# Kernel tuning notes

Hardware: AMD Instinct MI355X
Metric: run time of the kernel (lower is better)

Reference implementation:

```python
import jax, jax.numpy as jnp
import numpy as np

B, S, HIDDEN = 2, 2048, 2048
HEADS, GROUPS, KVC = 16, 4, 128
HPG = HEADS // GROUPS  # heads per group
LAYER_INDEX = 2
SOFTMAX_SCALE = KVC ** -0.5
ROPE_THETA = 10000.0


def _rope_tables(seq_len, dim, dtype=jnp.float32):
    inv_freq = 1.0 / (ROPE_THETA ** (jnp.arange(0, dim, 2, dtype=jnp.float32) / dim))
    t = jnp.arange(seq_len, dtype=jnp.float32)
    freqs = jnp.outer(t, inv_freq)  # [S, dim/2]
    return jnp.cos(freqs).astype(dtype), jnp.sin(freqs).astype(dtype)


def _apply_rope(x, cos, sin):
    # x: [b, s, h, d]; rotate-half (GPT-NeoX style)
    d2 = x.shape[-1] // 2
    x1, x2 = x[..., :d2], x[..., d2:]
    c = cos[None, :, None, :]
    s = sin[None, :, None, :]
    return jnp.concatenate([x1 * c - x2 * s, x2 * c + x1 * s], axis=-1)


def setup_inputs() -> dict:
    key = jax.random.key(0)
    k1, k2, k3, k4 = jax.random.split(key, 4)
    std = HIDDEN ** -0.5
    return {
        "x": jax.random.normal(k1, (B, S, HIDDEN), dtype=jnp.float32),
        "w_q": jax.random.normal(k2, (HIDDEN, HEADS * KVC), dtype=jnp.float32) * std,
        "w_kv": jax.random.normal(k3, (HIDDEN, 2 * GROUPS * KVC), dtype=jnp.float32) * std,
        "w_dense": jax.random.normal(k4, (HEADS * KVC, HIDDEN), dtype=jnp.float32) * std,
    }


def reference(x, w_q, w_kv, w_dense):
    b, s, _ = x.shape
    # QKV projections
    q = (x @ w_q).reshape(b, s, HEADS, KVC)                 # [b,s,H,d]
    kv = (x @ w_kv).reshape(b, s, 2, GROUPS, KVC)
    k, v = kv[:, :, 0], kv[:, :, 1]                          # [b,s,G,d]
    # Rotary embeddings on q and k
    cos, sin = _rope_tables(s, KVC, x.dtype)
    q = _apply_rope(q, cos, sin)
    k = _apply_rope(k, cos, sin)
    # GQA attention with per-layer scaling trick:
    # scores computed at scale/softmax of layer_index, cast fp32, rescaled back.
    qg = q.reshape(b, s, GROUPS, HPG, KVC)
    scores = jnp.einsum("bqghd,bkgd->bghqk", qg, k) * (SOFTMAX_SCALE / LAYER_INDEX)
    scores = scores.astype(jnp.float32) * LAYER_INDEX
    # causal mask
    causal = jnp.tril(jnp.ones((s, s), dtype=bool))
    mask_value = jnp.finfo(jnp.float32).min
    scores = jnp.where(causal[None, None, None, :, :], scores, mask_value)
    probs = jax.nn.softmax(scores, axis=-1).astype(x.dtype)  # dropout p=0 (eval)
    ctx = jnp.einsum("bghqk,bkgd->bqghd", probs, v).reshape(b, s, HEADS * KVC)
    return ctx @ w_dense
```

## Files before the change

kernel.cpp:

```cpp
#include <hip/hip_runtime.h>
#include <hip/hip_bf16.h>
#include <stdint.h>

typedef unsigned short u16;
typedef __bf16 bf16x8 __attribute__((ext_vector_type(8)));
typedef float f32x4 __attribute__((ext_vector_type(4)));

#define S_LEN 2048
#define BATCH 2
#define NHEADS 16
#define NGROUPS 4
#define DHEAD 128
#define QKV_W 3072

__device__ __forceinline__ float bf2f(u16 u) {
  union { uint32_t i; float f; } v; v.i = ((uint32_t)u) << 16; return v.f;
}
__device__ __forceinline__ u16 f2bf(float f) {
  union { float f; uint32_t i; } v; v.f = f;
  uint32_t r = v.i + 0x7FFF + ((v.i >> 16) & 1);
  return (u16)(r >> 16);
}
__device__ __forceinline__ void llds16(const void* g, void* l) {
  __builtin_amdgcn_global_load_lds(
      (const __attribute__((address_space(1))) uint32_t*)g,
      (__attribute__((address_space(3))) uint32_t*)l, 16, 0, 0);
}

__device__ __forceinline__ void store_out(u16* C, long i, float v) { C[i] = f2bf(v); }
__device__ __forceinline__ void store_out(float* C, long i, float v) { C[i] = v; }

__global__ void rope_tables_k(float* __restrict__ cosT, float* __restrict__ sinT) {
  int i = blockIdx.x * 256 + threadIdx.x;
  int s = i >> 6, j = i & 63;
  float inv = exp2f(-(float)j * 0.20762050593045983f);
  float ang = (float)s * inv;
  float sv, cv;
  sincosf(ang, &sv, &cv);
  cosT[i] = cv; sinT[i] = sv;
}

__global__ void cvt_f32_bf16(const float* __restrict__ in, u16* __restrict__ out) {
  long i = ((long)blockIdx.x * 256 + threadIdx.x) * 4;
  float4 v = *(const float4*)(in + i);
  ushort4 o;
  o.x = f2bf(v.x); o.y = f2bf(v.y); o.z = f2bf(v.z); o.w = f2bf(v.w);
  *(ushort4*)(out + i) = o;
}

__global__ void transpose_f32_bf16(const float* __restrict__ in, u16* __restrict__ out,
                                   int R, int C) {
  __shared__ u16 tile[32][33];
  int c0 = blockIdx.x * 32, r0 = blockIdx.y * 32;
  int tx = threadIdx.x, ty = threadIdx.y;
  for (int i = 0; i < 32; i += 8)
    tile[ty + i][tx] = f2bf(in[(long)(r0 + ty + i) * C + c0 + tx]);
  __syncthreads();
  for (int i = 0; i < 32; i += 8)
    out[(long)(c0 + ty + i) * R + r0 + tx] = tile[tx][ty + i];
}

template <typename OutT>
__global__ __launch_bounds__(256) void gemm_bt(
    const u16* __restrict__ A, const u16* __restrict__ Bt, OutT* __restrict__ C,
    int M, int N, int K) {
  __shared__ __align__(16) __bf16 As[128 * 32];
  __shared__ __align__(16) __bf16 Bs[128 * 32];
  const int tid = threadIdx.x;
  const int wv = tid >> 6;
  const int lane = tid & 63;
  const int quad = lane >> 4;
  const int l16 = lane & 15;
  const int bm = blockIdx.y * 128;
  const int bn = blockIdx.x * 128;

  f32x4 acc[4][4] = {};

  const int arow = wv * 32 + (lane >> 2);
  const int kseg = (lane & 3) * 8;
  const int wm = (wv >> 1) * 64, wn = (wv & 1) * 64;

  for (int k0 = 0; k0 < K; k0 += 32) {
    __syncthreads();
    const u16* ga0 = A + (long)(bm + arow) * K + k0 + kseg;
    llds16(ga0, &As[arow * 32 + kseg]);
    llds16(ga0 + (long)16 * K, &As[(arow + 16) * 32 + kseg]);
    const u16* gb0 = Bt + (long)(bn + arow) * K + k0 + kseg;
    llds16(gb0, &Bs[arow * 32 + kseg]);
    llds16(gb0 + (long)16 * K, &Bs[(arow + 16) * 32 + kseg]);
    __syncthreads();

    bf16x8 af[4], bfr[4];
#pragma unroll
    for (int mt = 0; mt < 4; ++mt)
      af[mt] = *(const bf16x8*)&As[(wm + mt * 16 + l16) * 32 + quad * 8];
#pragma unroll
    for (int nt = 0; nt < 4; ++nt)
      bfr[nt] = *(const bf16x8*)&Bs[(wn + nt * 16 + l16) * 32 + quad * 8];
#pragma unroll
    for (int mt = 0; mt < 4; ++mt)
#pragma unroll
      for (int nt = 0; nt < 4; ++nt)
        acc[mt][nt] = __builtin_amdgcn_mfma_f32_16x16x32_bf16(
            af[mt], bfr[nt], acc[mt][nt], 0, 0, 0);
  }

#pragma unroll
  for (int mt = 0; mt < 4; ++mt)
#pragma unroll
    for (int nt = 0; nt < 4; ++nt)
#pragma unroll
      for (int r = 0; r < 4; ++r) {
        int row = bm + wm + mt * 16 + quad * 4 + r;
        int col = bn + wn + nt * 16 + l16;
        store_out(C, (long)row * N + col, acc[mt][nt][r]);
      }
}

__global__ void rope_q_k(u16* __restrict__ qkv, const float* __restrict__ cosT,
                         const float* __restrict__ sinT) {
  long i = (long)blockIdx.x * 256 + threadIdx.x;
  int j = i & 63;
  long rest = i >> 6;
  int h = rest & 15;
  long bs = rest >> 4;
  int s = bs & (S_LEN - 1);
  long base = bs * QKV_W + h * DHEAD + j;
  float x1 = bf2f(qkv[base]), x2 = bf2f(qkv[base + 64]);
  float c = cosT[s * 64 + j], sn = sinT[s * 64 + j];
  qkv[base] = f2bf(x1 * c - x2 * sn);
  qkv[base + 64] = f2bf(x2 * c + x1 * sn);
}

__global__ void rope_k_k(const u16* __restrict__ qkv, u16* __restrict__ Kb,
                         const float* __restrict__ cosT, const float* __restrict__ sinT) {
  long i = (long)blockIdx.x * 256 + threadIdx.x;
  int j = i & 63;
  long rest = i >> 6;
  int g = rest & 3;
  long bs = rest >> 2;
  int s = bs & (S_LEN - 1);
  int b = (int)(bs >> 11);
  long src = bs * QKV_W + 2048 + g * 128 + j;
  float x1 = bf2f(qkv[src]), x2 = bf2f(qkv[src + 64]);
  float c = cosT[s * 64 + j], sn = sinT[s * 64 + j];
  long dst = ((long)(b * NGROUPS + g) * S_LEN + s) * DHEAD + j;
  Kb[dst] = f2bf(x1 * c - x2 * sn);
  Kb[dst + 64] = f2bf(x2 * c + x1 * sn);
}

__global__ void v_trans_k(const u16* __restrict__ qkv, u16* __restrict__ Vt) {
  __shared__ u16 tile[32][33];
  int s0 = blockIdx.x * 32, d0 = blockIdx.y * 32;
  int bg = blockIdx.z;
  int b = bg >> 2, g = bg & 3;
  int tx = threadIdx.x, ty = threadIdx.y;
  for (int i = 0; i < 32; i += 8) {
    long s = s0 + ty + i;
    tile[ty + i][tx] = qkv[((long)b * S_LEN + s) * QKV_W + 2560 + g * 128 + d0 + tx];
  }
  __syncthreads();
  for (int i = 0; i < 32; i += 8) {
    int d = d0 + ty + i;
    Vt[((long)(b * NGROUPS + g) * DHEAD + d) * S_LEN + s0 + tx] = tile[tx][ty + i];
  }
}

__global__ __launch_bounds__(256, 2) void attn_k5(
    const u16* __restrict__ Q,
    const u16* __restrict__ Kb,
    const u16* __restrict__ Vt,
    u16* __restrict__ ctx) {
  __shared__ __align__(16) __bf16 Ks[2][64 * 128];
  __shared__ __align__(16) __bf16 Vts[2][128 * 64];
  __shared__ __align__(16) __bf16 Ps[64 * 64];

  const int h = blockIdx.y, b = blockIdx.z, g = h >> 2;
  const int tid = threadIdx.x, wv = tid >> 6, lane = tid & 63;
  const int quad = lane >> 4, l16 = lane & 15;
  const float SCALE = 0.08838834764831845f;

  const long kbase = (long)(b * NGROUPS + g) * S_LEN * DHEAD;
  const long vbase = (long)(b * NGROUPS + g) * DHEAD * S_LEN;

  const int krow_off = lane >> 4;
  const int vrow_off = lane >> 3;

  const __bf16 oneb = (__bf16)((l16 == 0) ? 1.0f : 0.0f);
  const bf16x8 bones = {oneb, oneb, oneb, oneb, oneb, oneb, oneb, oneb};

  for (int pass = 0; pass < 2; ++pass) {
    const int tile = pass == 0 ? (int)blockIdx.x : 31 - (int)blockIdx.x;
    const int q0 = tile * 64;
    const int nch = tile + 1;

    bf16x8 aq[4];
    {
      const u16* qp = Q + (long)(b * S_LEN + q0 + wv * 16 + l16) * QKV_W + h * DHEAD + quad * 8;
#pragma unroll
      for (int ds = 0; ds < 4; ++ds)
        aq[ds] = *(const bf16x8*)(qp + ds * 32);
    }

#pragma unroll
    for (int i = 0; i < 4; ++i) {
      int r0 = wv * 16 + i * 4;
      int row = r0 + krow_off;
      int c = l16 ^ (row & 15);
      llds16(Kb + kbase + (long)row * DHEAD + c * 8, &Ks[0][r0 * 128 + lane * 8]);
    }
#pragma unroll
    for (int i = 0; i < 4; ++i) {
      int d0 = wv * 32 + i * 8;
      int row = d0 + vrow_off;
      int c = (lane & 7) ^ (row & 7);
      llds16(Vt + vbase + (long)row * S_LEN + c * 8, &Vts[0][d0 * 64 + lane * 8]);
    }
    __syncthreads();

    f32x4 Oacc[9] = {};

    for (int kc = 0; kc < nch; ++kc) {
      const int cur = kc & 1;
      if (kc + 1 < nch) {
        const int nxt = cur ^ 1;
#pragma unroll
        for (int i = 0; i < 4; ++i) {
          int r0 = wv * 16 + i * 4;
          int row = r0 + krow_off;
          int c = l16 ^ (row & 15);
          llds16(Kb + kbase + (long)((kc + 1) * 64 + row) * DHEAD + c * 8,
                 &Ks[nxt][r0 * 128 + lane * 8]);
        }
#pragma unroll
        for (int i = 0; i < 4; ++i) {
          int d0 = wv * 32 + i * 8;
          int row = d0 + vrow_off;
          int c = (lane & 7) ^ (row & 7);
          llds16(Vt + vbase + (long)row * S_LEN + (kc + 1) * 64 + c * 8,
                 &Vts[nxt][d0 * 64 + lane * 8]);
        }
      }

      f32x4 sacc[4] = {};
#pragma unroll
      for (int ds = 0; ds < 4; ++ds) {
        int pos0 = ((ds * 4 + quad) ^ l16) * 8;
#pragma unroll
        for (int nt = 0; nt < 4; ++nt) {
          bf16x8 bk = *(const bf16x8*)&Ks[cur][(nt * 16 + l16) * 128 + pos0];
          sacc[nt] = __builtin_amdgcn_mfma_f32_16x16x32_bf16(aq[ds], bk, sacc[nt], 0, 0, 0);
        }
      }

#pragma unroll
      for (int nt = 0; nt < 4; ++nt)
#pragma unroll
        for (int r = 0; r < 4; ++r) {
          int qrow = q0 + wv * 16 + quad * 4 + r;
          int key = kc * 64 + nt * 16 + l16;
          float p = (key <= qrow) ? __expf(sacc[nt][r] * SCALE) : 0.f;
          int qlocal = quad * 4 + r;
          int chunk = nt * 2 + (l16 >> 3);
          int pos = chunk ^ (qlocal & 7);
          Ps[(wv * 16 + qlocal) * 64 + pos * 8 + (l16 & 7)] = (__bf16)p;
        }

      bf16x8 ap[2];
#pragma unroll
      for (int kf = 0; kf < 2; ++kf) {
        int pos = ((kf * 4 + quad) ^ (l16 & 7)) * 8;
        ap[kf] = *(const bf16x8*)&Ps[(wv * 16 + l16) * 64 + pos];
      }
#pragma unroll
      for (int nt = 0; nt < 8; ++nt)
#pragma unroll
        for (int kf = 0; kf < 2; ++kf) {
          int pos = ((kf * 4 + quad) ^ (l16 & 7)) * 8;
          bf16x8 bv = *(const bf16x8*)&Vts[cur][(nt * 16 + l16) * 64 + pos];
          Oacc[nt] = __builtin_amdgcn_mfma_f32_16x16x32_bf16(ap[kf], bv, Oacc[nt], 0, 0, 0);
        }
      Oacc[8] = __builtin_amdgcn_mfma_f32_16x16x32_bf16(ap[0], bones, Oacc[8], 0, 0, 0);
      Oacc[8] = __builtin_amdgcn_mfma_f32_16x16x32_bf16(ap[1], bones, Oacc[8], 0, 0, 0);

      __syncthreads();
    }

    float lsum[4];
#pragma unroll
    for (int r = 0; r < 4; ++r)
      lsum[r] = __shfl(Oacc[8][r], quad << 4, 64);

    const long obase = ((long)(b * S_LEN + q0 + wv * 16) * NHEADS + h) * DHEAD;
#pragma unroll
    for (int nt = 0; nt < 8; ++nt)
#pragma unroll
      for (int r = 0; r < 4; ++r) {
        int lrow = quad * 4 + r;
        ctx[obase + (long)lrow * NHEADS * DHEAD + nt * 16 + l16] =
            f2bf(Oacc[nt][r] / lsum[r]);
      }
  }
}

extern "C" void kernel_launch(void* const* d_in, const int* in_sizes, int n_in,
                              void* d_out, int out_size, void* d_ws, size_t ws_size,
                              hipStream_t stream) {
  const float* x   = (const float*)d_in[0];
  const float* wq  = (const float*)d_in[1];
  const float* wkv = (const float*)d_in[2];
  const float* wd  = (const float*)d_in[3];
  float* out = (float*)d_out;

  char* ws = (char*)d_ws;
  float* cosT  = (float*)(ws + 0);
  float* sinT  = (float*)(ws + 524288);
  u16* wqkvT = (u16*)(ws + 1048576);
  u16* wdT   = (u16*)(ws + 13631488);
  u16* xb    = (u16*)(ws + 22020096);
  u16* qkv   = (u16*)(ws + 38797312);
  u16* Kb    = (u16*)(ws + 63963136);
  u16* Vt    = (u16*)(ws + 68157440);
  u16* ctx   = (u16*)(ws + 72351744);

  rope_tables_k<<<512, 256, 0, stream>>>(cosT, sinT);
  cvt_f32_bf16<<<8192, 256, 0, stream>>>(x, xb);
  transpose_f32_bf16<<<dim3(64, 64), dim3(32, 8), 0, stream>>>(wq, wqkvT, 2048, 2048);
  transpose_f32_bf16<<<dim3(32, 64), dim3(32, 8), 0, stream>>>(wkv, wqkvT + (long)2048 * 2048, 2048, 1024);
  transpose_f32_bf16<<<dim3(64, 64), dim3(32, 8), 0, stream>>>(wd, wdT, 2048, 2048);

  gemm_bt<u16><<<dim3(24, 32), 256, 0, stream>>>(xb, wqkvT, qkv, 4096, 3072, 2048);

  rope_q_k<<<16384, 256, 0, stream>>>(qkv, cosT, sinT);
  rope_k_k<<<4096, 256, 0, stream>>>(qkv, Kb, cosT, sinT);
  v_trans_k<<<dim3(64, 4, 8), dim3(32, 8), 0, stream>>>(qkv, Vt);

  attn_k5<<<dim3(16, 16, 2), 256, 0, stream>>>(qkv, Kb, Vt, ctx);

  gemm_bt<float><<<dim3(16, 32), 256, 0, stream>>>(ctx, wdT, out, 4096, 2048, 2048);
}
```

Before: 313.3 us.

## Replace GEMM with 256x256 double-buffered, swizzled 8-wave pipelined kernel

Replaces the 128x128 single-buffered GEMM with a 512-thread kernel computing 256x256 tiles. K-steps are 64 wide, held in double-buffered LDS with an XOR-swizzled layout, and staged with global_load_lds prefetch two steps ahead. Each K-step is split into four phases with barriers and s_setprio so loads overlap MFMA work, and the workgroup index is remapped for cache locality. The aim is to hide global memory latency and raise reuse, at the cost of fewer workgroups (192 and 128 tiles on the MI355X's CUs) and heavier register and LDS use.

```diff
diff --git a/kernel.cpp b/kernel.cpp
--- a/kernel.cpp
+++ b/kernel.cpp
@@ -60,60 +60,162 @@
     out[(long)(c0 + ty + i) * R + r0 + tx] = tile[tx][ty + i];
 }
 
+
+#define GFENCE() asm volatile("" ::: "memory")
+#define MIDBAR() do { GFENCE(); __builtin_amdgcn_s_barrier(); \
+    asm volatile("s_waitcnt lgkmcnt(0)" ::: "memory"); } while (0)
+#define ENDBAR() do { GFENCE(); __builtin_amdgcn_s_barrier(); GFENCE(); } while (0)
+
+__device__ __forceinline__ bf16x8 frag_ld(const __bf16* h, int wrow, int kk, int quad) {
+  int b = ((wrow & 15) << 6) | (quad << 4);
+  b ^= ((wrow >> 3) & 1) << 5;
+  int off = ((((wrow >> 4) << 1) | kk) << 10) | b;
+  return *(const bf16x8*)((const char*)h + off);
+}
+
+__device__ __forceinline__ void stage_half(const u16* __restrict__ g, int K,
+                                           __bf16* lhalf, int wv, int lane) {
+  int bsrc = (lane << 4) ^ (((lane >> 5) & 1) << 5);
+  int r = bsrc >> 6, c = (bsrc & 63) >> 1;
+  int cb = (wv & 1) << 5;
+  llds16(g + (long)((wv >> 1) * 16 + r) * K + cb + c,
+         lhalf + wv * 512 + lane * 8);
+  llds16(g + (long)((4 + (wv >> 1)) * 16 + r) * K + cb + c,
+         lhalf + 4096 + wv * 512 + lane * 8);
+}
+
 template <typename OutT>
-__global__ __launch_bounds__(256) void gemm_bt(
+__global__ __launch_bounds__(512) void gemm_bt8(
     const u16* __restrict__ A, const u16* __restrict__ Bt, OutT* __restrict__ C,
     int M, int N, int K) {
-  __shared__ __align__(16) __bf16 As[128 * 32];
-  __shared__ __align__(16) __bf16 Bs[128 * 32];
+  __shared__ __align__(16) __bf16 lds[2][2][16384];
   const int tid = threadIdx.x;
-  const int wv = tid >> 6;
-  const int lane = tid & 63;
-  const int quad = lane >> 4;
-  const int l16 = lane & 15;
-  const int bm = blockIdx.y * 128;
-  const int bn = blockIdx.x * 128;
-
-  f32x4 acc[4][4] = {};
-
-  const int arow = wv * 32 + (lane >> 2);
-  const int kseg = (lane & 3) * 8;
-  const int wm = (wv >> 1) * 64, wn = (wv & 1) * 64;
-
-  for (int k0 = 0; k0 < K; k0 += 32) {
-    __syncthreads();
-    const u16* ga0 = A + (long)(bm + arow) * K + k0 + kseg;
-    llds16(ga0, &As[arow * 32 + kseg]);
-    llds16(ga0 + (long)16 * K, &As[(arow + 16) * 32 + kseg]);
-    const u16* gb0 = Bt + (long)(bn + arow) * K + k0 + kseg;
-    llds16(gb0, &Bs[arow * 32 + kseg]);
-    llds16(gb0 + (long)16 * K, &Bs[(arow + 16) * 32 + kseg]);
-    __syncthreads();
-
-    bf16x8 af[4], bfr[4];
-#pragma unroll
-    for (int mt = 0; mt < 4; ++mt)
-      af[mt] = *(const bf16x8*)&As[(wm + mt * 16 + l16) * 32 + quad * 8];
+  const int wv = tid >> 6, lane = tid & 63;
+  const int quad = lane >> 4, l16 = lane & 15;
+  const int wr = wv >> 2, wc = wv & 3;
+
+  const int nwg = gridDim.x * gridDim.y;
+  const int orig = blockIdx.y * gridDim.x + blockIdx.x;
+  const int swz = (orig & 7) * (nwg >> 3) + (orig >> 3);
+  const int bx = swz % gridDim.x, by = swz / gridDim.x;
+  const int bm = by * 256, bn = bx * 256;
+
+  const u16* Abase = A + (long)bm * K;
+  const u16* Bbase = Bt + (long)bn * K;
+  const int NT = K >> 6;
+
+  f32x4 acc[8][4] = {};
+
+  stage_half(Abase, K, &lds[0][0][0], wv, lane);
+  stage_half(Abase + (long)128 * K, K, &lds[0][0][8192], wv, lane);
+  stage_half(Bbase, K, &lds[0][1][0], wv, lane);
+  stage_half(Bbase + (long)128 * K, K, &lds[0][1][8192], wv, lane);
+  stage_half(Abase + 64, K, &lds[1][0][0], wv, lane);
+  stage_half(Abase + (long)128 * K + 64, K, &lds[1][0][8192], wv, lane);
+  stage_half(Bbase + 64, K, &lds[1][1][0], wv, lane);
+  stage_half(Bbase + (long)128 * K + 64, K, &lds[1][1][8192], wv, lane);
+  asm volatile("s_waitcnt vmcnt(8)" ::: "memory");
+  __builtin_amdgcn_s_barrier();
+  GFENCE();
+
+  for (int kt = 0; kt < NT; ++kt) {
+    const int buf = kt & 1;
+    const __bf16* Ah = &lds[buf][0][wr * 8192];
+    const __bf16* Bh = &lds[buf][1][(wc >> 1) * 8192];
+    const int brow0 = (wc & 1) << 6;
+    const bool pre = (kt + 2 < NT);
+    bf16x8 aF[4][2], bF[4][2];
+
+#pragma unroll
+    for (int m = 0; m < 4; ++m) {
+      aF[m][0] = frag_ld(Ah, m * 16 + l16, 0, quad);
+      aF[m][1] = frag_ld(Ah, m * 16 + l16, 1, quad);
+    }
+#pragma unroll
+    for (int n = 0; n < 2; ++n) {
+      bF[n][0] = frag_ld(Bh, brow0 + n * 16 + l16, 0, quad);
+      bF[n][1] = frag_ld(Bh, brow0 + n * 16 + l16, 1, quad);
+    }
+    MIDBAR();
+    __builtin_amdgcn_s_setprio(1);
+#pragma unroll
+    for (int m = 0; m < 4; ++m)
+#pragma unroll
+      for (int n = 0; n < 2; ++n) {
+        acc[m][n] = __builtin_amdgcn_mfma_f32_16x16x32_bf16(aF[m][0], bF[n][0], acc[m][n], 0, 0, 0);
+        acc[m][n] = __builtin_amdgcn_mfma_f32_16x16x32_bf16(aF[m][1], bF[n][1], acc[m][n], 0, 0, 0);
+      }
+    __builtin_amdgcn_s_setprio(0);
+    ENDBAR();
+
+#pragma unroll
+    for (int n = 2; n < 4; ++n) {
+      bF[n][0] = frag_ld(Bh, brow0 + n * 16 + l16, 0, quad);
+      bF[n][1] = frag_ld(Bh, brow0 + n * 16 + l16, 1, quad);
+    }
+    MIDBAR();
+    __builtin_amdgcn_s_setprio(1);
+#pragma unroll
+    for (int m = 0; m < 4; ++m)
+#pragma unroll
+      for (int n = 2; n < 4; ++n) {
+        acc[m][n] = __builtin_amdgcn_mfma_f32_16x16x32_bf16(aF[m][0], bF[n][0], acc[m][n], 0, 0, 0);
+        acc[m][n] = __builtin_amdgcn_mfma_f32_16x16x32_bf16(aF[m][1], bF[n][1], acc[m][n], 0, 0, 0);
+      }
+    __builtin_amdgcn_s_setprio(0);
+    ENDBAR();
+
+#pragma unroll
+    for (int m = 0; m < 4; ++m) {
+      aF[m][0] = frag_ld(Ah, 64 + m * 16 + l16, 0, quad);
+      aF[m][1] = frag_ld(Ah, 64 + m * 16 + l16, 1, quad);
+    }
+    if (pre) {
+      const u16* p = Bbase + (long)(kt + 2) * 64;
+      stage_half(p, K, &lds[buf][1][0], wv, lane);
+      stage_half(p + (long)128 * K, K, &lds[buf][1][8192], wv, lane);
+    }
+    MIDBAR();
+    __builtin_amdgcn_s_setprio(1);
+#pragma unroll
+    for (int m = 0; m < 4; ++m)
+#pragma unroll
+      for (int n = 2; n < 4; ++n) {
+        acc[4 + m][n] = __builtin_amdgcn_mfma_f32_16x16x32_bf16(aF[m][0], bF[n][0], acc[4 + m][n], 0, 0, 0);
+        acc[4 + m][n] = __builtin_amdgcn_mfma_f32_16x16x32_bf16(aF[m][1], bF[n][1], acc[4 + m][n], 0, 0, 0);
+      }
+    __builtin_amdgcn_s_setprio(0);
+    ENDBAR();
+
+    if (pre) {
+      const u16* p = Abase + (long)(kt + 2) * 64;
+      stage_half(p, K, &lds[buf][0][0], wv, lane);
+      stage_half(p + (long)128 * K, K, &lds[buf][0][8192], wv, lane);
+    }
+    MIDBAR();
+    __builtin_amdgcn_s_setprio(1);
+#pragma unroll
+    for (int m = 0; m < 4; ++m)
+#pragma unroll
+      for (int n = 0; n < 2; ++n) {
+        acc[4 + m][n] = __builtin_amdgcn_mfma_f32_16x16x32_bf16(aF[m][0], bF[n][0], acc[4 + m][n], 0, 0, 0);
+        acc[4 + m][n] = __builtin_amdgcn_mfma_f32_16x16x32_bf16(aF[m][1], bF[n][1], acc[4 + m][n], 0, 0, 0);
+      }
+    __builtin_amdgcn_s_setprio(0);
+    if (pre) { asm volatile("s_waitcnt vmcnt(8)" ::: "memory"); }
+    else     { asm volatile("s_waitcnt vmcnt(0)" ::: "memory"); }
+    ENDBAR();
+  }
+
+  const long colbase = (long)bn + wc * 64 + l16;
+#pragma unroll
+  for (int mt = 0; mt < 8; ++mt)
 #pragma unroll
     for (int nt = 0; nt < 4; ++nt)
-      bfr[nt] = *(const bf16x8*)&Bs[(wn + nt * 16 + l16) * 32 + quad * 8];
-#pragma unroll
-    for (int mt = 0; mt < 4; ++mt)
-#pragma unroll
-      for (int nt = 0; nt < 4; ++nt)
-        acc[mt][nt] = __builtin_amdgcn_mfma_f32_16x16x32_bf16(
-            af[mt], bfr[nt], acc[mt][nt], 0, 0, 0);
-  }
-
-#pragma unroll
-  for (int mt = 0; mt < 4; ++mt)
-#pragma unroll
-    for (int nt = 0; nt < 4; ++nt)
-#pragma unroll
-      for (int r = 0; r < 4; ++r) {
-        int row = bm + wm + mt * 16 + quad * 4 + r;
-        int col = bn + wn + nt * 16 + l16;
-        store_out(C, (long)row * N + col, acc[mt][nt][r]);
+#pragma unroll
+      for (int rr = 0; rr < 4; ++rr) {
+        long row = bm + wr * 128 + mt * 16 + quad * 4 + rr;
+        store_out(C, row * N + colbase + nt * 16, acc[mt][nt][rr]);
       }
 }
 
@@ -329,7 +431,7 @@
   transpose_f32_bf16<<<dim3(32, 64), dim3(32, 8), 0, stream>>>(wkv, wqkvT + (long)2048 * 2048, 2048, 1024);
   transpose_f32_bf16<<<dim3(64, 64), dim3(32, 8), 0, stream>>>(wd, wdT, 2048, 2048);
 
-  gemm_bt<u16><<<dim3(24, 32), 256, 0, stream>>>(xb, wqkvT, qkv, 4096, 3072, 2048);
+  gemm_bt8<u16><<<dim3(12, 16), 512, 0, stream>>>(xb, wqkvT, qkv, 4096, 3072, 2048);
 
   rope_q_k<<<16384, 256, 0, stream>>>(qkv, cosT, sinT);
   rope_k_k<<<4096, 256, 0, stream>>>(qkv, Kb, cosT, sinT);
@@ -337,5 +439,5 @@
 
   attn_k5<<<dim3(16, 16, 2), 256, 0, stream>>>(qkv, Kb, Vt, ctx);
 
-  gemm_bt<float><<<dim3(16, 32), 256, 0, stream>>>(ctx, wdT, out, 4096, 2048, 2048);
-}
+  gemm_bt8<float><<<dim3(8, 16), 512, 0, stream>>>(ctx, wdT, out, 4096, 2048, 2048);
+}
```

Measured after the change: 319.1 us. Within noise of the previous version (+1.9%).
